# Performance work log

Hardware: AMD Instinct MI355X
Metric: run time of the kernel (lower is better)

The kernel has to match this reference:

```python
import jax, jax.numpy as jnp
import numpy as np
from jax import lax

B, T, D, H, L, W = 256, 1024, 32, 64, 32, 64
DT0 = 0.4  # fixed dt0 in _sample


def _u(key, shape, fan_in):
    lim = 1.0 / np.sqrt(fan_in)
    return jax.random.uniform(key, shape, dtype=jnp.float32, minval=-lim, maxval=lim)


def setup_inputs() -> dict:
    key = jax.random.key(0)
    ks = jax.random.split(key, 32)
    inp = {}
    inp['ts'] = jnp.sort(jax.random.uniform(ks[0], (B, T), dtype=jnp.float32) * 10.0, axis=1)
    inp['ys'] = jax.random.normal(ks[1], (B, T, D), dtype=jnp.float32)
    inp['eps'] = jax.random.normal(ks[2], (B, L), dtype=jnp.float32)
    inp['scale'] = jnp.ones(())
    # Func MLP: H -> W -> W -> H, softplus hidden acts, tanh final
    inp['fw0'] = _u(ks[3], (W, H), H); inp['fb0'] = _u(ks[4], (W,), H)
    inp['fw1'] = _u(ks[5], (W, W), W); inp['fb1'] = _u(ks[6], (W,), W)
    inp['fw2'] = _u(ks[7], (H, W), W); inp['fb2'] = _u(ks[8], (H,), W)
    # GRUCell: input D+1 (time concat), hidden H (equinox layout)
    inp['gru_wi'] = _u(ks[9], (3 * H, D + 1), D + 1)
    inp['gru_wh'] = _u(ks[10], (3 * H, H), H)
    inp['gru_b'] = _u(ks[11], (3 * H,), H)
    inp['gru_bn'] = _u(ks[12], (H,), H)
    inp['hl_w'] = _u(ks[13], (2 * L, H), H); inp['hl_b'] = _u(ks[14], (2 * L,), H)
    # latent_to_hidden MLP: L -> W -> W -> H, relu hidden (equinox default), identity final
    inp['lh_w0'] = _u(ks[15], (W, L), L); inp['lh_b0'] = _u(ks[16], (W,), L)
    inp['lh_w1'] = _u(ks[17], (W, W), W); inp['lh_b1'] = _u(ks[18], (W,), W)
    inp['lh_w2'] = _u(ks[19], (H, W), W); inp['lh_b2'] = _u(ks[20], (H,), W)
    inp['hd_w'] = _u(ks[21], (D, H), H); inp['hd_b'] = _u(ks[22], (D,), H)
    return inp


def _forward(ts, ys, eps, scale, fw0, fb0, fw1, fb1, fw2, fb2,
             gru_wi, gru_wh, gru_b, gru_bn, hl_w, hl_b,
             lh_w0, lh_b0, lh_w1, lh_b1, lh_w2, lh_b2, hd_w, hd_b):
    Bv, Tlen = ts.shape
    Hv = gru_wh.shape[1]
    Lv = hl_w.shape[0] // 2

    # ---- encoder: GRU over reversed (t, y) sequence ----
    data = jnp.concatenate([ts[..., None], ys], axis=-1)    # [B,T,D+1]
    data_rev = jnp.swapaxes(data[:, ::-1, :], 0, 1)          # [T,B,D+1]

    def gru_step(h, x):
        ig = x @ gru_wi.T + gru_b                            # [B,3H]
        hg = h @ gru_wh.T                                    # [B,3H]
        ir, iz, inn = jnp.split(ig, 3, axis=-1)
        hr, hz, hn = jnp.split(hg, 3, axis=-1)
        r = jax.nn.sigmoid(ir + hr)
        z = jax.nn.sigmoid(iz + hz)
        n = jnp.tanh(inn + r * (hn + gru_bn))
        return n + z * (h - n), None

    hidden, _ = lax.scan(gru_step, jnp.zeros((Bv, Hv), data.dtype), data_rev)

    context = hidden @ hl_w.T + hl_b                         # [B,2L]
    mean, logstd = context[:, :Lv], context[:, Lv:]
    std = jnp.exp(logstd)
    latent = mean + eps * std                                # reparameterized sample

    # ---- latent -> initial hidden state (relu MLP) ----
    h0 = jax.nn.relu(latent @ lh_w0.T + lh_b0)
    h0 = jax.nn.relu(h0 @ lh_w1.T + lh_b1)
    y0 = h0 @ lh_w2.T + lh_b2                                # [B,H]

    def func(y):  # Func: scale * mlp(y); softplus hidden, tanh final
        a = jax.nn.softplus(y @ fw0.T + fb0)
        a = jax.nn.softplus(a @ fw1.T + fb1)
        return scale * jnp.tanh(a @ fw2.T + fb2)

    # ---- Euler integrator over T steps (vector field is time-independent) ----
    def euler_step(carry, _):
        t0, y = carry
        y1 = y + DT0 * func(y)
        return (t0 + DT0, y1), y1

    (_, _), ys_h = lax.scan(euler_step, (ts[:, 0], y0), None, length=Tlen)  # [T,B,H]
    pred_ys = jnp.swapaxes(ys_h @ hd_w.T + hd_b, 0, 1)       # [B,T,D]

    # ---- ELBO-style loss, per sample ----
    recon = 0.5 * jnp.sum((ys - pred_ys) ** 2, axis=(1, 2))
    kl = 0.5 * jnp.sum(mean ** 2 + std ** 2 - 2.0 * jnp.log(std) - 1.0, axis=1)
    return recon + kl                                         # [B]


def reference(ts, ys, eps, scale, fw0, fb0, fw1, fb1, fw2, fb2,
              gru_wi, gru_wh, gru_b, gru_bn, hl_w, hl_b,
              lh_w0, lh_b0, lh_w1, lh_b1, lh_w2, lh_b2, hd_w, hd_b):
    return _forward(ts, ys, eps, scale, fw0, fb0, fw1, fb1, fw2, fb2,
                    gru_wi, gru_wh, gru_b, gru_bn, hl_w, hl_b,
                    lh_w0, lh_b0, lh_w1, lh_b1, lh_w2, lh_b2, hd_w, hd_b)
```

## Files before the change

### kernel.cpp

```cpp
#include <hip/hip_runtime.h>
#include <math.h>

#define NB 256
#define NT 1024
#define ND 32
#define NH 64
#define NL 32
#define DT0 0.4f
#define XB 36

__device__ __forceinline__ float dot4(float4 a, float4 b) {
    return a.x * b.x + a.y * b.y + a.z * b.z + a.w * b.w;
}
__device__ __forceinline__ float fsigm(float x) {
    return __fdividef(1.0f, 1.0f + __expf(-x));
}
__device__ __forceinline__ float ftanh(float x) {
    float cx = fminf(fmaxf(x, -15.0f), 15.0f);
    float e2 = __expf(2.0f * cx);
    return __fdividef(e2 - 1.0f, e2 + 1.0f);
}
__device__ __forceinline__ float fsoftplus(float x) {
    return fmaxf(x, 0.0f) + __logf(1.0f + __expf(-fabsf(x)));
}

template <int CTRL>
__device__ __forceinline__ float dpp_add(float x) {
    int t = __builtin_amdgcn_update_dpp(0, __float_as_int(x), CTRL, 0xF, 0xF, true);
    return x + __int_as_float(t);
}
__device__ __forceinline__ float quad_reduce(float x) {
    x = dpp_add<0xB1>(x);
    x = dpp_add<0x4E>(x);
    return x;
}
__device__ __forceinline__ float red8(float x) {
    x = dpp_add<0xB1>(x);
    x = dpp_add<0x4E>(x);
    x = dpp_add<0x104>(x);
    return x;
}

extern "C" __global__ void __launch_bounds__(256, 1)
latentode_fused(const float* __restrict__ ts,
                const float* __restrict__ ys,
                const float* __restrict__ eps,
                const float* __restrict__ scale_p,
                const float* __restrict__ fw0, const float* __restrict__ fb0,
                const float* __restrict__ fw1, const float* __restrict__ fb1,
                const float* __restrict__ fw2, const float* __restrict__ fb2,
                const float* __restrict__ gwi, const float* __restrict__ gwh,
                const float* __restrict__ gb,  const float* __restrict__ gbn,
                const float* __restrict__ hlw, const float* __restrict__ hlb,
                const float* __restrict__ lw0, const float* __restrict__ lb0,
                const float* __restrict__ lw1, const float* __restrict__ lb1,
                const float* __restrict__ lw2, const float* __restrict__ lb2,
                const float* __restrict__ hdw, const float* __restrict__ hdb,
                float* __restrict__ out)
{
    const int b   = blockIdx.x;
    const int tid = threadIdx.x;

    __shared__ __align__(16) float xb[(NT + 2) * XB];
    __shared__ __align__(16) float hbuf[2][64];
    __shared__ __align__(16) float a0b[64];
    __shared__ __align__(16) float a1b[64];
    __shared__ __align__(16) float tmpb[64];
    __shared__ __align__(16) float ybuf[64];
    __shared__ __align__(16) float latb[32];
    __shared__ float redr[32];

    for (int i = tid; i < NT * 8; i += 256) {
        const int row = i >> 3, q = i & 7;
        *(float4*)&xb[row * XB + q * 4] =
            *(const float4*)(ys + (size_t)(b * NT + row) * ND + q * 4);
    }
    for (int i = tid; i < NT; i += 256) xb[i * XB + 32] = ts[b * NT + i];

    const int u = tid >> 2;
    const int p = tid & 3;
    const float4* whr = (const float4*)(gwh + (u)       * 64 + p * 16);
    const float4* whz = (const float4*)(gwh + (64 + u)  * 64 + p * 16);
    const float4* whn = (const float4*)(gwh + (128 + u) * 64 + p * 16);
    const float4 WR0=whr[0], WR1=whr[1], WR2=whr[2], WR3=whr[3];
    const float4 WZ0=whz[0], WZ1=whz[1], WZ2=whz[2], WZ3=whz[3];
    const float4 WN0=whn[0], WN1=whn[1], WN2=whn[2], WN3=whn[3];
    const float* gr = gwi + u * 33;
    const float* gz = gwi + (64 + u) * 33;
    const float* gn = gwi + (128 + u) * 33;
    const int o = 8 * p;
    const float4 RIA = make_float4(gr[1+o], gr[2+o], gr[3+o], gr[4+o]);
    const float4 RIB = make_float4(gr[5+o], gr[6+o], gr[7+o], gr[8+o]);
    const float4 ZIA = make_float4(gz[1+o], gz[2+o], gz[3+o], gz[4+o]);
    const float4 ZIB = make_float4(gz[5+o], gz[6+o], gz[7+o], gz[8+o]);
    const float4 NIA = make_float4(gn[1+o], gn[2+o], gn[3+o], gn[4+o]);
    const float4 NIB = make_float4(gn[5+o], gn[6+o], gn[7+o], gn[8+o]);
    const float RT  = (p == 0) ? gr[0] : 0.0f;
    const float ZT  = (p == 0) ? gz[0] : 0.0f;
    const float NTW = (p == 0) ? gn[0] : 0.0f;
    const float gbr_ = gb[u], gbz_ = gb[64 + u], gbn_ = gb[128 + u];
    const float bnv  = gbn[u];

    if (tid < 64) hbuf[0][tid] = 0.0f;
    __syncthreads();

    float hreg = 0.0f;
    float4 xA = *(const float4*)(&xb[0] + o);
    float4 xB = *(const float4*)(&xb[0] + o + 4);
    float tsv = xb[32];

#define GRU_STEP(SROW, RD, WR)                                                  \
    {                                                                           \
        const float* xrown = &xb[((SROW) + 1) * XB];                            \
        const float4 nxA = *(const float4*)(xrown + o);                         \
        const float4 nxB = *(const float4*)(xrown + o + 4);                     \
        const float ntsv = xrown[32];                                           \
        const float4* hv = (const float4*)&hbuf[RD][p * 16];                    \
        const float4 h0 = hv[0], h1 = hv[1], h2 = hv[2], h3 = hv[3];            \
        float ar = dot4(WR0,h0) + dot4(WR1,h1) + dot4(WR2,h2) + dot4(WR3,h3)    \
                 + dot4(RIA,xA) + dot4(RIB,xB) + RT * tsv;                      \
        float az = dot4(WZ0,h0) + dot4(WZ1,h1) + dot4(WZ2,h2) + dot4(WZ3,h3)    \
                 + dot4(ZIA,xA) + dot4(ZIB,xB) + ZT * tsv;                      \
        float ahn = dot4(WN0,h0) + dot4(WN1,h1) + dot4(WN2,h2) + dot4(WN3,h3);  \
        float ain = dot4(NIA,xA) + dot4(NIB,xB) + NTW * tsv;                    \
        ar  = quad_reduce(ar);                                                  \
        az  = quad_reduce(az);                                                  \
        ahn = quad_reduce(ahn);                                                 \
        ain = quad_reduce(ain);                                                 \
        const float rg = fsigm(ar + gbr_);                                      \
        const float zg = fsigm(az + gbz_);                                      \
        const float ng = ftanh(ain + gbn_ + rg * (ahn + bnv));                  \
        hreg = ng + zg * (hreg - ng);                                           \
        if (p == 0) hbuf[WR][u] = hreg;                                         \
        xA = nxA; xB = nxB; tsv = ntsv;                                         \
        __syncthreads();                                                        \
    }

    for (int s = 0; s < NT; s += 2) {
        GRU_STEP(s,     0, 1);
        GRU_STEP(s + 1, 1, 0);
    }

    if (tid < 64) {
        const float4* wp = (const float4*)(hlw + tid * 64);
        const float4* hv = (const float4*)&hbuf[0][0];
        float a0 = hlb[tid], a1 = 0.0f;
#pragma unroll
        for (int q = 0; q < 16; q += 2) { a0 += dot4(wp[q], hv[q]); a1 += dot4(wp[q+1], hv[q+1]); }
        tmpb[tid] = a0 + a1;
    }
    __syncthreads();
    float klpart = 0.0f;
    if (tid < 32) {
        const float mean   = tmpb[tid];
        const float logstd = tmpb[32 + tid];
        const float stdv   = __expf(logstd);
        latb[tid] = mean + eps[b * NL + tid] * stdv;
        klpart = 0.5f * (mean * mean + stdv * stdv - 2.0f * logstd - 1.0f);
    }
    __syncthreads();
    if (tid < 64) {
        const float4* wp = (const float4*)(lw0 + tid * 32);
        const float4* lv = (const float4*)latb;
        float a0 = lb0[tid], a1 = 0.0f;
#pragma unroll
        for (int q = 0; q < 8; q += 2) { a0 += dot4(wp[q], lv[q]); a1 += dot4(wp[q+1], lv[q+1]); }
        a0b[tid] = fmaxf(a0 + a1, 0.0f);
    }
    __syncthreads();
    if (tid < 64) {
        const float4* wp = (const float4*)(lw1 + tid * 64);
        const float4* av = (const float4*)a0b;
        float a0 = lb1[tid], a1 = 0.0f;
#pragma unroll
        for (int q = 0; q < 16; q += 2) { a0 += dot4(wp[q], av[q]); a1 += dot4(wp[q+1], av[q+1]); }
        a1b[tid] = fmaxf(a0 + a1, 0.0f);
    }
    __syncthreads();
    if (tid < 64) {
        const float4* wp = (const float4*)(lw2 + tid * 64);
        const float4* tv = (const float4*)a1b;
        float a0 = lb2[tid], a1 = 0.0f;
#pragma unroll
        for (int q = 0; q < 16; q += 2) { a0 += dot4(wp[q], tv[q]); a1 += dot4(wp[q+1], tv[q+1]); }
        ybuf[tid] = a0 + a1;
    }
    __syncthreads();

    const int er = tid >> 2, ep = tid & 3;
    const int hb2 = (tid >> 2) & 1;
    const int hp = (ep << 1) | hb2;
    const int hr = tid >> 3;
    const float4* q0 = (const float4*)(fw0 + er * 64 + ep * 16);
    const float4 E00=q0[0], E01=q0[1], E02=q0[2], E03=q0[3];
    const float4* q1 = (const float4*)(fw1 + er * 64 + ep * 16);
    const float4 E10=q1[0], E11=q1[1], E12=q1[2], E13=q1[3];
    const float4* q2 = (const float4*)(fw2 + er * 64 + ep * 16);
    const float4 E20=q2[0], E21=q2[1], E22=q2[2], E23=q2[3];
    const float b0 = fb0[er], b1 = fb1[er], b2 = fb2[er];
    const float4* qh = (const float4*)(hdw + hr * 64 + hp * 8);
    const float4 HD0 = qh[0], HD1 = qh[1];
    const float hdbias = hdb[hr];
    const float dts = DT0 * scale_p[0];
    float ylocal = (ep == 0) ? ybuf[er] : 0.0f;
    float rec = 0.0f;

#define EULER_STEP(SS, DO_REC)                                                  \
    {                                                                           \
        const float4* yv = (const float4*)ybuf;                                 \
        const float4 ya0 = yv[ep*4+0], ya1 = yv[ep*4+1],                        \
                     ya2 = yv[ep*4+2], ya3 = yv[ep*4+3];                        \
        {                                                                       \
            float l0 = dot4(E00, ya0) + dot4(E01, ya1)                          \
                     + dot4(E02, ya2) + dot4(E03, ya3);                         \
            l0 = quad_reduce(l0);                                               \
            if (ep == 0) a0b[er] = fsoftplus(l0 + b0);                          \
        }                                                                       \
        __syncthreads();                                                        \
        {                                                                       \
            const float4* av = (const float4*)a0b;                              \
            float l1 = dot4(E10, av[ep*4+0]) + dot4(E11, av[ep*4+1])            \
                     + dot4(E12, av[ep*4+2]) + dot4(E13, av[ep*4+3]);           \
            l1 = quad_reduce(l1);                                               \
            const float4 za = hb2 ? ya2 : ya0;                                  \
            const float4 zb = hb2 ? ya3 : ya1;                                  \
            float ph = dot4(HD0, za) + dot4(HD1, zb);                           \
            ph = red8(ph);                                                      \
            if (ep == 0) a1b[er] = fsoftplus(l1 + b1);                          \
            if (DO_REC && (tid & 7) == 0) {                                     \
                const float d = xb[((SS) - 1) * XB + hr] - (ph + hdbias);       \
                rec += d * d;                                                   \
            }                                                                   \
        }                                                                       \
        __syncthreads();                                                        \
        {                                                                       \
            const float4* bv = (const float4*)a1b;                              \
            float l2 = dot4(E20, bv[ep*4+0]) + dot4(E21, bv[ep*4+1])            \
                     + dot4(E22, bv[ep*4+2]) + dot4(E23, bv[ep*4+3]);           \
            l2 = quad_reduce(l2);                                               \
            if (ep == 0) {                                                      \
                ylocal += dts * ftanh(l2 + b2);                                 \
                ybuf[er] = ylocal;                                              \
            }                                                                   \
        }                                                                       \
        __syncthreads();                                                        \
    }

    EULER_STEP(0, false);
    for (int s = 1; s < NT - 1; s += 2) {
        EULER_STEP(s,     true);
        EULER_STEP(s + 1, true);
    }
    EULER_STEP(NT - 1, true);

    {
        const float4* yv = (const float4*)ybuf;
        const float4 za = yv[hp*2+0], zb = yv[hp*2+1];
        float ph = dot4(HD0, za) + dot4(HD1, zb);
        ph = red8(ph);
        if ((tid & 7) == 0) {
            const float d = xb[(NT - 1) * XB + hr] - (ph + hdbias);
            rec += d * d;
            redr[hr] = rec;
        }
    }
    float klv = klpart;
    klv += __shfl_xor(klv, 1);
    klv += __shfl_xor(klv, 2);
    klv += __shfl_xor(klv, 4);
    klv += __shfl_xor(klv, 8);
    klv += __shfl_xor(klv, 16);
    __syncthreads();
    if (tid == 0) {
        float rs = 0.0f;
#pragma unroll
        for (int k2 = 0; k2 < 32; ++k2) rs += redr[k2];
        out[b] = 0.5f * rs + klv;
    }
}

extern "C" void kernel_launch(void* const* d_in, const int* in_sizes, int n_in,
                              void* d_out, int out_size, void* d_ws, size_t ws_size,
                              hipStream_t stream) {
    (void)in_sizes; (void)n_in; (void)out_size; (void)d_ws; (void)ws_size;
    const float* ts      = (const float*)d_in[0];
    const float* ys      = (const float*)d_in[1];
    const float* eps     = (const float*)d_in[2];
    const float* scale_p = (const float*)d_in[3];
    const float* fw0     = (const float*)d_in[4];
    const float* fb0     = (const float*)d_in[5];
    const float* fw1     = (const float*)d_in[6];
    const float* fb1     = (const float*)d_in[7];
    const float* fw2     = (const float*)d_in[8];
    const float* fb2     = (const float*)d_in[9];
    const float* gwi     = (const float*)d_in[10];
    const float* gwh     = (const float*)d_in[11];
    const float* gbv     = (const float*)d_in[12];
    const float* gbn     = (const float*)d_in[13];
    const float* hlw     = (const float*)d_in[14];
    const float* hlb     = (const float*)d_in[15];
    const float* lw0     = (const float*)d_in[16];
    const float* lb0     = (const float*)d_in[17];
    const float* lw1     = (const float*)d_in[18];
    const float* lb1     = (const float*)d_in[19];
    const float* lw2     = (const float*)d_in[20];
    const float* lb2     = (const float*)d_in[21];
    const float* hdw     = (const float*)d_in[22];
    const float* hdb     = (const float*)d_in[23];
    float* out = (float*)d_out;

    hipLaunchKernelGGL(latentode_fused, dim3(NB), dim3(256), 0, stream,
                       ts, ys, eps, scale_p, fw0, fb0, fw1, fb1, fw2, fb2,
                       gwi, gwh, gbv, gbn, hlw, hlb, lw0, lb0, lw1, lb1,
                       lw2, lb2, hdw, hdb, out);
}
```

Before: 1.070 ms.

## Run Euler recurrence in a single wavefront without block barriers

Moves the per-step MLP recurrence onto one 64-lane wavefront, where each lane owns a full output row with its weights held in registers. This removes the three block-wide barriers and the cross-lane DPP reductions per step, at the cost of four times more serial FMAs per lane and much higher register use. It relies on wave-level ordering of LDS accesses instead of explicit synchronization.

```diff
diff --git a/kernel.cpp b/kernel.cpp
--- a/kernel.cpp
+++ b/kernel.cpp
@@ -32,12 +32,6 @@
 __device__ __forceinline__ float quad_reduce(float x) {
     x = dpp_add<0xB1>(x);
     x = dpp_add<0x4E>(x);
-    return x;
-}
-__device__ __forceinline__ float red8(float x) {
-    x = dpp_add<0xB1>(x);
-    x = dpp_add<0x4E>(x);
-    x = dpp_add<0x104>(x);
     return x;
 }
 
@@ -187,83 +181,88 @@
     }
     __syncthreads();
 
-    const int er = tid >> 2, ep = tid & 3;
-    const int hb2 = (tid >> 2) & 1;
-    const int hp = (ep << 1) | hb2;
-    const int hr = tid >> 3;
-    const float4* q0 = (const float4*)(fw0 + er * 64 + ep * 16);
-    const float4 E00=q0[0], E01=q0[1], E02=q0[2], E03=q0[3];
-    const float4* q1 = (const float4*)(fw1 + er * 64 + ep * 16);
-    const float4 E10=q1[0], E11=q1[1], E12=q1[2], E13=q1[3];
-    const float4* q2 = (const float4*)(fw2 + er * 64 + ep * 16);
-    const float4 E20=q2[0], E21=q2[1], E22=q2[2], E23=q2[3];
-    const float b0 = fb0[er], b1 = fb1[er], b2 = fb2[er];
-    const float4* qh = (const float4*)(hdw + hr * 64 + hp * 8);
-    const float4 HD0 = qh[0], HD1 = qh[1];
-    const float hdbias = hdb[hr];
     const float dts = DT0 * scale_p[0];
-    float ylocal = (ep == 0) ? ybuf[er] : 0.0f;
-    float rec = 0.0f;
-
-#define EULER_STEP(SS, DO_REC)                                                  \
-    {                                                                           \
-        const float4* yv = (const float4*)ybuf;                                 \
-        const float4 ya0 = yv[ep*4+0], ya1 = yv[ep*4+1],                        \
-                     ya2 = yv[ep*4+2], ya3 = yv[ep*4+3];                        \
-        {                                                                       \
-            float l0 = dot4(E00, ya0) + dot4(E01, ya1)                          \
-                     + dot4(E02, ya2) + dot4(E03, ya3);                         \
-            l0 = quad_reduce(l0);                                               \
-            if (ep == 0) a0b[er] = fsoftplus(l0 + b0);                          \
-        }                                                                       \
-        __syncthreads();                                                        \
-        {                                                                       \
-            const float4* av = (const float4*)a0b;                              \
-            float l1 = dot4(E10, av[ep*4+0]) + dot4(E11, av[ep*4+1])            \
-                     + dot4(E12, av[ep*4+2]) + dot4(E13, av[ep*4+3]);           \
-            l1 = quad_reduce(l1);                                               \
-            const float4 za = hb2 ? ya2 : ya0;                                  \
-            const float4 zb = hb2 ? ya3 : ya1;                                  \
-            float ph = dot4(HD0, za) + dot4(HD1, zb);                           \
-            ph = red8(ph);                                                      \
-            if (ep == 0) a1b[er] = fsoftplus(l1 + b1);                          \
-            if (DO_REC && (tid & 7) == 0) {                                     \
-                const float d = xb[((SS) - 1) * XB + hr] - (ph + hdbias);       \
-                rec += d * d;                                                   \
-            }                                                                   \
-        }                                                                       \
-        __syncthreads();                                                        \
-        {                                                                       \
-            const float4* bv = (const float4*)a1b;                              \
-            float l2 = dot4(E20, bv[ep*4+0]) + dot4(E21, bv[ep*4+1])            \
-                     + dot4(E22, bv[ep*4+2]) + dot4(E23, bv[ep*4+3]);           \
-            l2 = quad_reduce(l2);                                               \
-            if (ep == 0) {                                                      \
-                ylocal += dts * ftanh(l2 + b2);                                 \
-                ybuf[er] = ylocal;                                              \
-            }                                                                   \
-        }                                                                       \
-        __syncthreads();                                                        \
-    }
-
-    EULER_STEP(0, false);
-    for (int s = 1; s < NT - 1; s += 2) {
-        EULER_STEP(s,     true);
-        EULER_STEP(s + 1, true);
-    }
-    EULER_STEP(NT - 1, true);
-
-    {
-        const float4* yv = (const float4*)ybuf;
-        const float4 za = yv[hp*2+0], zb = yv[hp*2+1];
-        float ph = dot4(HD0, za) + dot4(HD1, zb);
-        ph = red8(ph);
-        if ((tid & 7) == 0) {
-            const float d = xb[(NT - 1) * XB + hr] - (ph + hdbias);
-            rec += d * d;
-            redr[hr] = rec;
+    if (tid < 64) {
+        const int ln = tid;
+        const int hrow = ln >> 1, hh = ln & 1;
+        float4 F0[16], F1[16], F2[16], HDh[8];
+        {
+            const float4* pf0 = (const float4*)(fw0 + ln * 64);
+            const float4* pf1 = (const float4*)(fw1 + ln * 64);
+            const float4* pf2 = (const float4*)(fw2 + ln * 64);
+            const float4* phd = (const float4*)(hdw + hrow * 64 + hh * 32);
+#pragma unroll
+            for (int q = 0; q < 16; ++q) { F0[q] = pf0[q]; F1[q] = pf1[q]; F2[q] = pf2[q]; }
+#pragma unroll
+            for (int q = 0; q < 8; ++q) HDh[q] = phd[q];
         }
-    }
+        const float eb0 = fb0[ln], eb1 = fb1[ln], eb2 = fb2[ln];
+        const float hdbias = hdb[hrow];
+        float yreg = ybuf[ln];
+        float rec = 0.0f;
+
+        for (int s = 0; s < NT; ++s) {
+            {
+                const float4* yv = (const float4*)ybuf;
+                float la = 0.f, lb = 0.f, lc = 0.f, ld = 0.f;
+#pragma unroll
+                for (int q = 0; q < 16; q += 4) {
+                    la += dot4(F0[q+0], yv[q+0]);
+                    lb += dot4(F0[q+1], yv[q+1]);
+                    lc += dot4(F0[q+2], yv[q+2]);
+                    ld += dot4(F0[q+3], yv[q+3]);
+                }
+                a0b[ln] = fsoftplus((la + lb) + (lc + ld) + eb0);
+                const float4* yh = (const float4*)(ybuf + hh * 32);
+                float hdp = 0.f;
+#pragma unroll
+                for (int j = 0; j < 8; ++j) hdp += dot4(HDh[j], yh[j]);
+                hdp = dpp_add<0xB1>(hdp);
+                if (hh == 0 && s > 0) {
+                    const float d = xb[(s - 1) * XB + hrow] - (hdp + hdbias);
+                    rec += d * d;
+                }
+            }
+            {
+                const float4* av = (const float4*)a0b;
+                float la = 0.f, lb = 0.f, lc = 0.f, ld = 0.f;
+#pragma unroll
+                for (int q = 0; q < 16; q += 4) {
+                    la += dot4(F1[q+0], av[q+0]);
+                    lb += dot4(F1[q+1], av[q+1]);
+                    lc += dot4(F1[q+2], av[q+2]);
+                    ld += dot4(F1[q+3], av[q+3]);
+                }
+                a1b[ln] = fsoftplus((la + lb) + (lc + ld) + eb1);
+            }
+            {
+                const float4* bv = (const float4*)a1b;
+                float la = 0.f, lb = 0.f, lc = 0.f, ld = 0.f;
+#pragma unroll
+                for (int q = 0; q < 16; q += 4) {
+                    la += dot4(F2[q+0], bv[q+0]);
+                    lb += dot4(F2[q+1], bv[q+1]);
+                    lc += dot4(F2[q+2], bv[q+2]);
+                    ld += dot4(F2[q+3], bv[q+3]);
+                }
+                yreg += dts * ftanh((la + lb) + (lc + ld) + eb2);
+                ybuf[ln] = yreg;
+            }
+        }
+        {
+            const float4* yh = (const float4*)(ybuf + hh * 32);
+            float hdp = 0.f;
+#pragma unroll
+            for (int j = 0; j < 8; ++j) hdp += dot4(HDh[j], yh[j]);
+            hdp = dpp_add<0xB1>(hdp);
+            if (hh == 0) {
+                const float d = xb[(NT - 1) * XB + hrow] - (hdp + hdbias);
+                rec += d * d;
+                redr[hrow] = rec;
+            }
+        }
+    }
+
     float klv = klpart;
     klv += __shfl_xor(klv, 1);
     klv += __shfl_xor(klv, 2);
```

Result: slower. 1.795 ms (+67.8%).
